# Kernel tuning notes

Hardware: AMD Instinct MI355X
Metric: run time of the kernel (lower is better)

The kernel has to match this reference:

```python
import jax, jax.numpy as jnp
import numpy as np
from jax.scipy.special import xlogy

W_BI = 0.5
W_TRI = 0.5
EPS = 1e-10


def setup_inputs() -> dict:
    key = jax.random.key(0)
    B, L, V = 8, 2048, 512
    logits = jax.random.normal(key, (B, L, V), dtype=jnp.float32)
    return {"logits": logits}


def _safe_normalized_entropy(joint, max_log):
    # 1 - H(joint)/H_max (concentration penalty), fp32-safe
    joint = joint / (joint.sum() + EPS)
    entropy = -xlogy(joint, jnp.clip(joint, EPS, None)).sum()
    return jnp.clip(1.0 - entropy / (max_log + EPS), 0.0, 1.0)


def reference(logits):
    x = jnp.nan_to_num(logits.astype(jnp.float32), nan=0.0, posinf=80.0, neginf=-80.0)
    p = jax.nn.softmax(x, axis=-1)  # (B, L, V)
    B, L, V = p.shape
    max_log_bi = float(np.log(float(V * V)))
    max_log_tri = float(np.log(float(V) ** 3))

    total = jnp.zeros((), dtype=jnp.float32)

    # Bigram joint distribution over (V, V)
    bigram_joint = jnp.einsum('nla,nlb->ab', p[:, :-1, :], p[:, 1:, :])
    total = total + W_BI * _safe_normalized_entropy(bigram_joint, max_log_bi)

    # Trigram: (V,V) bigram part outer-producted with third-position marginal -> (V,V,V)
    bi_part = jnp.einsum('nla,nlb->ab', p[:, :-2, :], p[:, 1:-1, :])
    tri_joint = jnp.einsum('ab,nlc->abc', bi_part, p[:, 2:, :])
    total = total + W_TRI * _safe_normalized_entropy(tri_joint, max_log_tri)

    return jnp.clip(jnp.nan_to_num(total, nan=0.0, posinf=1.0), 0.0, 1.0)
```

## Files before the change

### kernel.cpp

```cpp
#include <hip/hip_runtime.h>
#include <math.h>

#define L_SEQ 2048
#define V 512
#define NROWS 16384
#define LDT 16448
#define NSPLIT 32
#define EPS 1e-10

typedef __bf16 bf16x8 __attribute__((ext_vector_type(8)));
typedef float f32x4 __attribute__((ext_vector_type(4)));

#define PT_OFF  ((size_t)0)
#define GP_OFF  ((size_t)512 * LDT * 2)
#define RB_OFF  (GP_OFF + (size_t)NSPLIT * V * V * 4)
#define M_OFF   (RB_OFF + (size_t)23 * V * 4)
#define PC_OFF  (M_OFF + (size_t)V * 4)

#define GLDS16(g, l) __builtin_amdgcn_global_load_lds( \
    (const __attribute__((address_space(1))) unsigned int*)(g), \
    (__attribute__((address_space(3))) unsigned int*)(l), 16, 0, 0)

__device__ __forceinline__ unsigned short f2bf(float f) {
    unsigned u = __float_as_uint(f);
    unsigned r = (u + 0x7fffu + ((u >> 16) & 1u)) >> 16;
    return (unsigned short)r;
}

__device__ __forceinline__ void softmax_row_bf16(const float* __restrict__ x,
                                                 int lane, unsigned short* out) {
    float4 va = *(const float4*)(x + lane * 4);
    float4 vb = *(const float4*)(x + 256 + lane * 4);
    float v[8] = {va.x, va.y, va.z, va.w, vb.x, vb.y, vb.z, vb.w};
    float e[8];
    float s = 0.0f;
#pragma unroll
    for (int i = 0; i < 8; i++) {
        float xi = fminf(fmaxf(v[i], -80.0f), 80.0f);
        e[i] = __expf(xi);
        s += e[i];
    }
#pragma unroll
    for (int o = 32; o; o >>= 1) s += __shfl_xor(s, o, 64);
    float inv = 1.0f / s;
#pragma unroll
    for (int i = 0; i < 8; i++) out[i] = f2bf(e[i] * inv);
}

__global__ __launch_bounds__(256) void softmaxT_k(const float* __restrict__ in,
                                                  unsigned short* __restrict__ pT,
                                                  float* __restrict__ rb) {
    __shared__ __align__(16) unsigned short sm[32 * 512];
    int t = threadIdx.x;
    int w = t >> 6, lane = t & 63;
    if (blockIdx.x >= 512) {
        int j = blockIdx.x - 512;
        if (w == 0) {
            int r = j < 8 ? j * L_SEQ + L_SEQ - 2
                  : j < 16 ? (j - 8) * L_SEQ + L_SEQ - 1
                  : (j - 15) * L_SEQ;
            unsigned short o[8];
            softmax_row_bf16(in + (size_t)r * V, lane, o);
#pragma unroll
            for (int i = 0; i < 4; i++)
                rb[j * V + lane * 4 + i] = __uint_as_float((unsigned)o[i] << 16);
#pragma unroll
            for (int i = 0; i < 4; i++)
                rb[j * V + 256 + lane * 4 + i] = __uint_as_float((unsigned)o[4 + i] << 16);
        }
        return;
    }
    int k0 = blockIdx.x * 32;
#pragma unroll
    for (int i = 0; i < 8; i++) {
        int rr = w * 8 + i;
        unsigned short o[8];
        softmax_row_bf16(in + (size_t)(k0 + rr) * V, lane, o);
        *(ushort4*)&sm[rr * 512 + lane * 4] = make_ushort4(o[0], o[1], o[2], o[3]);
        *(ushort4*)&sm[rr * 512 + 256 + lane * 4] = make_ushort4(o[4], o[5], o[6], o[7]);
    }
    __syncthreads();
    int cA = 2 * t, cB = cA + 1;
    unsigned u[32];
#pragma unroll
    for (int k = 0; k < 32; k++) u[k] = *(const unsigned*)&sm[k * 512 + cA];
    unsigned oA[16], oB[16];
#pragma unroll
    for (int i = 0; i < 16; i++) {
        unsigned e0 = u[2 * i], e1 = u[2 * i + 1];
        oA[i] = (e0 & 0xffffu) | (e1 << 16);
        oB[i] = (e0 >> 16) | (e1 & 0xffff0000u);
    }
    uint4* dA = (uint4*)(pT + (size_t)cA * LDT + k0);
    uint4* dB = (uint4*)(pT + (size_t)cB * LDT + k0);
#pragma unroll
    for (int i = 0; i < 4; i++) {
        dA[i] = make_uint4(oA[4 * i], oA[4 * i + 1], oA[4 * i + 2], oA[4 * i + 3]);
        dB[i] = make_uint4(oB[4 * i], oB[4 * i + 1], oB[4 * i + 2], oB[4 * i + 3]);
    }
    if (blockIdx.x == 511) {
#pragma unroll
        for (int j = 0; j < 8; j++) {
            *(uint4*)(pT + (size_t)cA * LDT + 16384 + 8 * j) = make_uint4(0, 0, 0, 0);
            *(uint4*)(pT + (size_t)cB * LDT + 16384 + 8 * j) = make_uint4(0, 0, 0, 0);
        }
    }
}

__global__ __launch_bounds__(256) void gemm_k(const unsigned short* __restrict__ pT,
                                              float* __restrict__ gp) {
    __shared__ __align__(16) uint4 ldsA[512];
    __shared__ __align__(16) uint4 ldsB[512];
    int tile = blockIdx.x & 15, split = blockIdx.x >> 4;
    int ta = (tile >> 2) * 128, tb = (tile & 3) * 128;
    int t = threadIdx.x, w = t >> 6, lane = t & 63;
    int l15 = lane & 15, q = lane >> 4;
    int wa = (w & 1) * 64, wb = (w >> 1) * 64;
    int k0base = split * 512;

    f32x4 acc[4][4];
#pragma unroll
    for (int g = 0; g < 4; g++)
#pragma unroll
        for (int h = 0; h < 4; h++) acc[g][h] = (f32x4){0.f, 0.f, 0.f, 0.f};

    int srow = 16 * w + (lane >> 2);
    int qoff = (lane & 3) * 8;
    const size_t rA1 = (size_t)(ta + srow) * LDT;
    const size_t rA2 = (size_t)(ta + 64 + srow) * LDT;
    const size_t rB1 = (size_t)(tb + srow) * LDT;
    const size_t rB2 = (size_t)(tb + 64 + srow) * LDT;

    for (int it = 0; it < 16; it++) {
        int kel = k0base + it * 32 + qoff;
        const unsigned short* gb1 = pT + rB1 + kel;
        const unsigned short* gb2 = pT + rB2 + kel;
        uint4 x1 = *(const uint4*)gb1;
        unsigned y1 = *(const unsigned*)(gb1 + 8);
        uint4 x2 = *(const uint4*)gb2;
        unsigned y2 = *(const unsigned*)(gb2 + 8);
        __syncthreads();
        GLDS16(pT + rA1 + kel, &ldsA[64 * w]);
        GLDS16(pT + rA2 + kel, &ldsA[256 + 64 * w]);
        uint4 s1, s2;
        s1.x = (x1.x >> 16) | (x1.y << 16);
        s1.y = (x1.y >> 16) | (x1.z << 16);
        s1.z = (x1.z >> 16) | (x1.w << 16);
        s1.w = (x1.w >> 16) | (y1 << 16);
        s2.x = (x2.x >> 16) | (x2.y << 16);
        s2.y = (x2.y >> 16) | (x2.z << 16);
        s2.z = (x2.z >> 16) | (x2.w << 16);
        s2.w = (x2.w >> 16) | (y2 << 16);
        ldsB[64 * w + lane] = s1;
        ldsB[256 + 64 * w + lane] = s2;
        __syncthreads();
        bf16x8 af[4], bv[4];
#pragma unroll
        for (int g = 0; g < 4; g++)
            af[g] = __builtin_bit_cast(bf16x8, ldsA[4 * (wa + g * 16 + l15) + q]);
#pragma unroll
        for (int h = 0; h < 4; h++)
            bv[h] = __builtin_bit_cast(bf16x8, ldsB[4 * (wb + h * 16 + l15) + q]);
#pragma unroll
        for (int g = 0; g < 4; g++)
#pragma unroll
            for (int h = 0; h < 4; h++)
                acc[g][h] = __builtin_amdgcn_mfma_f32_16x16x32_bf16(af[g], bv[h], acc[g][h], 0, 0, 0);
    }

    float* og = gp + (size_t)split * V * V;
#pragma unroll
    for (int g = 0; g < 4; g++) {
        int a = ta + wa + g * 16 + q * 4;
#pragma unroll
        for (int h = 0; h < 4; h++) {
            int b = tb + wb + h * 16 + l15;
#pragma unroll
            for (int r = 0; r < 4; r++)
                og[(size_t)(a + r) * V + b] = acc[g][h][r];
        }
    }
}

__global__ __launch_bounds__(256) void reduce_k(const unsigned short* __restrict__ pT,
                                                const float* __restrict__ gp,
                                                const float* __restrict__ rb,
                                                float* __restrict__ m,
                                                double* __restrict__ pc) {
    int bid = blockIdx.x, t = threadIdx.x;
    if (bid < 512) {
        const unsigned short* row = pT + (size_t)bid * LDT;
        float s = 0.0f;
#pragma unroll
        for (int j = 0; j < 8; j++) {
            int g = t + 256 * j;
            uint4 x = *(const uint4*)(row + g * 8);
            float partial = 0.0f;
            unsigned ww[4] = {x.x, x.y, x.z, x.w};
#pragma unroll
            for (int qq = 0; qq < 4; qq++) {
                partial += __uint_as_float(ww[qq] << 16);
                partial += __uint_as_float(ww[qq] & 0xffff0000u);
            }
            if ((g & 255) == 0)
                partial -= __uint_as_float(ww[0] << 16) + __uint_as_float(ww[0] & 0xffff0000u);
            s += partial;
        }
#pragma unroll
        for (int o = 32; o; o >>= 1) s += __shfl_xor(s, o, 64);
        __shared__ float redc[4];
        if ((t & 63) == 0) redc[t >> 6] = s;
        __syncthreads();
        if (t == 0) m[bid] = redc[0] + redc[1] + redc[2] + redc[3];
    } else {
        int idx = (bid - 512) * 256 + t;
        int a = idx >> 9, b = idx & (V - 1);
        double ga = 0, gb2 = 0, gc = 0, gd = 0;
#pragma unroll
        for (int s = 0; s < NSPLIT; s += 4) {
            ga += (double)gp[(size_t)(s + 0) * V * V + idx];
            gb2 += (double)gp[(size_t)(s + 1) * V * V + idx];
            gc += (double)gp[(size_t)(s + 2) * V * V + idx];
            gd += (double)gp[(size_t)(s + 3) * V * V + idx];
        }
        double g = (ga + gb2) + (gc + gd);
        float cross = 0.f, cc = 0.f;
#pragma unroll
        for (int n = 0; n < 7; n++)
            cross = fmaf(rb[(8 + n) * V + a], rb[(16 + n) * V + b], cross);
#pragma unroll
        for (int n = 0; n < 8; n++)
            cc = fmaf(rb[n * V + a], rb[(8 + n) * V + b], cc);
        double g1 = g - (double)cross;
        double g2 = g1 - (double)cc;
        double s1 = g1, t1 = g1 * (double)logf((float)g1);
        double s2 = g2, t2 = g2 * (double)logf((float)g2);
#pragma unroll
        for (int o = 32; o; o >>= 1) {
            s1 += __shfl_xor(s1, o, 64);
            t1 += __shfl_xor(t1, o, 64);
            s2 += __shfl_xor(s2, o, 64);
            t2 += __shfl_xor(t2, o, 64);
        }
        __shared__ double redg[4][4];
        if ((t & 63) == 0) {
            int w = t >> 6;
            redg[w][0] = s1; redg[w][1] = t1; redg[w][2] = s2; redg[w][3] = t2;
        }
        __syncthreads();
        if (t == 0) {
            double* o = pc + (size_t)(bid - 512) * 4;
            o[0] = redg[0][0] + redg[1][0] + redg[2][0] + redg[3][0];
            o[1] = redg[0][1] + redg[1][1] + redg[2][1] + redg[3][1];
            o[2] = redg[0][2] + redg[1][2] + redg[2][2] + redg[3][2];
            o[3] = redg[0][3] + redg[1][3] + redg[2][3] + redg[3][3];
        }
    }
}

__global__ __launch_bounds__(512) void final_k(const float* __restrict__ m,
                                               const double* __restrict__ pc,
                                               float* __restrict__ out) {
    int t = threadIdx.x;
    double s1 = 0, t1 = 0, s2 = 0, t2 = 0;
#pragma unroll
    for (int j = 0; j < 2; j++) {
        const double* q = pc + (size_t)(t + 512 * j) * 4;
        s1 += q[0]; t1 += q[1]; s2 += q[2]; t2 += q[3];
    }
    double mv = (double)m[t];
    double sm = mv;
    double tm = mv * log(mv);
#pragma unroll
    for (int o = 32; o; o >>= 1) {
        sm += __shfl_xor(sm, o, 64);
        tm += __shfl_xor(tm, o, 64);
        s1 += __shfl_xor(s1, o, 64);
        t1 += __shfl_xor(t1, o, 64);
        s2 += __shfl_xor(s2, o, 64);
        t2 += __shfl_xor(t2, o, 64);
    }
    __shared__ double red[6][8];
    if ((t & 63) == 0) {
        int w = t >> 6;
        red[0][w] = sm; red[1][w] = tm;
        red[2][w] = s1; red[3][w] = t1;
        red[4][w] = s2; red[5][w] = t2;
    }
    __syncthreads();
    if (t == 0) {
        double acc[6];
        for (int i = 0; i < 6; i++) {
            acc[i] = 0;
            for (int w = 0; w < 8; w++) acc[i] += red[i][w];
        }
        double Sm = acc[0], Tm = acc[1];
        double S1 = acc[2], T1 = acc[3], S2 = acc[4], T2 = acc[5];
        double D1 = S1 + EPS;
        double Hbi = (log(D1) * S1 - T1) / D1;
        double mlb = log((double)V * (double)V);
        double cbi = 1.0 - Hbi / (mlb + EPS);
        cbi = fmin(fmax(cbi, 0.0), 1.0);
        double S3 = S2 * Sm;
        double D3 = S3 + EPS;
        double Htri = (log(D3) * S3 - (Sm * T2 + S2 * Tm)) / D3;
        double mlt = log((double)V * (double)V * (double)V);
        double ctri = 1.0 - Htri / (mlt + EPS);
        ctri = fmin(fmax(ctri, 0.0), 1.0);
        double tot = 0.5 * cbi + 0.5 * ctri;
        if (!(tot == tot)) tot = 0.0;
        tot = fmin(fmax(tot, 0.0), 1.0);
        out[0] = (float)tot;
    }
}

extern "C" void kernel_launch(void* const* d_in, const int* in_sizes, int n_in,
                              void* d_out, int out_size, void* d_ws, size_t ws_size,
                              hipStream_t stream) {
    (void)in_sizes; (void)n_in; (void)out_size; (void)ws_size;
    const float* logits = (const float*)d_in[0];
    float* out = (float*)d_out;
    char* ws = (char*)d_ws;
    unsigned short* pT = (unsigned short*)(ws + PT_OFF);
    float* gp = (float*)(ws + GP_OFF);
    float* rb = (float*)(ws + RB_OFF);
    float* m = (float*)(ws + M_OFF);
    double* pc = (double*)(ws + PC_OFF);

    softmaxT_k<<<535, 256, 0, stream>>>(logits, pT, rb);
    gemm_k<<<512, 256, 0, stream>>>(pT, gp);
    reduce_k<<<1536, 256, 0, stream>>>(pT, gp, rb, m, pc);
    final_k<<<1, 512, 0, stream>>>(m, pc, out);
}
```

Measured before the change: 114.9 us.

## Fuse column marginal partial sums into softmax and remap GEMM blocks per XCD

The softmax-transpose kernel now also computes per-block partial column sums of the bf16 probabilities, skipping the first two rows of each sequence, and writes them to a new workspace buffer. The reduce kernel combines these 512x512 partials instead of re-reading the whole 16 MB transposed probability matrix, which cuts its marginal-block count from 512 to 16. Separately, the GEMM block-to-(split, tile) mapping is changed so that each XCD handles contiguous K-splits, aiming for better L2 reuse of the A/B panels. The cost is an extra 1 MB write in the softmax kernel and a different floating-point summation order for the marginals.

New measurement: 114.0 us. No clear change (-0.7%).

```diff
diff --git a/kernel.cpp b/kernel.cpp
--- a/kernel.cpp
+++ b/kernel.cpp
@@ -16,6 +16,7 @@
 #define RB_OFF  (GP_OFF + (size_t)NSPLIT * V * V * 4)
 #define M_OFF   (RB_OFF + (size_t)23 * V * 4)
 #define PC_OFF  (M_OFF + (size_t)V * 4)
+#define MP_OFF  (PC_OFF + (size_t)1024 * 4 * 8)
 
 #define GLDS16(g, l) __builtin_amdgcn_global_load_lds( \
     (const __attribute__((address_space(1))) unsigned int*)(g), \
@@ -49,7 +50,8 @@
 
 __global__ __launch_bounds__(256) void softmaxT_k(const float* __restrict__ in,
                                                   unsigned short* __restrict__ pT,
-                                                  float* __restrict__ rb) {
+                                                  float* __restrict__ rb,
+                                                  float* __restrict__ mp) {
     __shared__ __align__(16) unsigned short sm[32 * 512];
     int t = threadIdx.x;
     int w = t >> 6, lane = t & 63;
@@ -84,6 +86,15 @@
     unsigned u[32];
 #pragma unroll
     for (int k = 0; k < 32; k++) u[k] = *(const unsigned*)&sm[k * 512 + cA];
+    bool excl = ((blockIdx.x & 63) == 0);
+    float mA = 0.0f, mB = 0.0f;
+#pragma unroll
+    for (int k = 0; k < 32; k++) {
+        if (excl && k < 2) continue;
+        mA += __uint_as_float(u[k] << 16);
+        mB += __uint_as_float(u[k] & 0xffff0000u);
+    }
+    *(float2*)&mp[(size_t)blockIdx.x * 512 + cA] = make_float2(mA, mB);
     unsigned oA[16], oB[16];
 #pragma unroll
     for (int i = 0; i < 16; i++) {
@@ -111,7 +122,10 @@
                                               float* __restrict__ gp) {
     __shared__ __align__(16) uint4 ldsA[512];
     __shared__ __align__(16) uint4 ldsB[512];
-    int tile = blockIdx.x & 15, split = blockIdx.x >> 4;
+    int b = blockIdx.x;
+    int xcd = b & 7, j = b >> 3;
+    int split = xcd * 4 + (j >> 4);
+    int tile = j & 15;
     int ta = (tile >> 2) * 128, tb = (tile & 3) * 128;
     int t = threadIdx.x, w = t >> 6, lane = t & 63;
     int l15 = lane & 15, q = lane >> 4;
@@ -174,46 +188,38 @@
         int a = ta + wa + g * 16 + q * 4;
 #pragma unroll
         for (int h = 0; h < 4; h++) {
-            int b = tb + wb + h * 16 + l15;
+            int b2 = tb + wb + h * 16 + l15;
 #pragma unroll
             for (int r = 0; r < 4; r++)
-                og[(size_t)(a + r) * V + b] = acc[g][h][r];
-        }
-    }
-}
-
-__global__ __launch_bounds__(256) void reduce_k(const unsigned short* __restrict__ pT,
+                og[(size_t)(a + r) * V + b2] = acc[g][h][r];
+        }
+    }
+}
+
+__global__ __launch_bounds__(256) void reduce_k(const float* __restrict__ mp,
                                                 const float* __restrict__ gp,
                                                 const float* __restrict__ rb,
                                                 float* __restrict__ m,
                                                 double* __restrict__ pc) {
     int bid = blockIdx.x, t = threadIdx.x;
-    if (bid < 512) {
-        const unsigned short* row = pT + (size_t)bid * LDT;
+    if (bid < 16) {
+        int c = bid * 32 + (t & 31);
+        int seg = t >> 5;
         float s = 0.0f;
 #pragma unroll
-        for (int j = 0; j < 8; j++) {
-            int g = t + 256 * j;
-            uint4 x = *(const uint4*)(row + g * 8);
-            float partial = 0.0f;
-            unsigned ww[4] = {x.x, x.y, x.z, x.w};
-#pragma unroll
-            for (int qq = 0; qq < 4; qq++) {
-                partial += __uint_as_float(ww[qq] << 16);
-                partial += __uint_as_float(ww[qq] & 0xffff0000u);
-            }
-            if ((g & 255) == 0)
-                partial -= __uint_as_float(ww[0] << 16) + __uint_as_float(ww[0] & 0xffff0000u);
-            s += partial;
-        }
-#pragma unroll
-        for (int o = 32; o; o >>= 1) s += __shfl_xor(s, o, 64);
-        __shared__ float redc[4];
-        if ((t & 63) == 0) redc[t >> 6] = s;
+        for (int i = 0; i < 64; i++)
+            s += mp[(size_t)(seg * 64 + i) * 512 + c];
+        __shared__ float redm[8][32];
+        redm[seg][t & 31] = s;
         __syncthreads();
-        if (t == 0) m[bid] = redc[0] + redc[1] + redc[2] + redc[3];
+        if (t < 32) {
+            float acc = 0.0f;
+#pragma unroll
+            for (int sgi = 0; sgi < 8; sgi++) acc += redm[sgi][t];
+            m[bid * 32 + t] = acc;
+        }
     } else {
-        int idx = (bid - 512) * 256 + t;
+        int idx = (bid - 16) * 256 + t;
         int a = idx >> 9, b = idx & (V - 1);
         double ga = 0, gb2 = 0, gc = 0, gd = 0;
 #pragma unroll
@@ -249,7 +255,7 @@
         }
         __syncthreads();
         if (t == 0) {
-            double* o = pc + (size_t)(bid - 512) * 4;
+            double* o = pc + (size_t)(bid - 16) * 4;
             o[0] = redg[0][0] + redg[1][0] + redg[2][0] + redg[3][0];
             o[1] = redg[0][1] + redg[1][1] + redg[2][1] + redg[3][1];
             o[2] = redg[0][2] + redg[1][2] + redg[2][2] + redg[3][2];
@@ -326,9 +332,10 @@
     float* rb = (float*)(ws + RB_OFF);
     float* m = (float*)(ws + M_OFF);
     double* pc = (double*)(ws + PC_OFF);
-
-    softmaxT_k<<<535, 256, 0, stream>>>(logits, pT, rb);
+    float* mp = (float*)(ws + MP_OFF);
+
+    softmaxT_k<<<535, 256, 0, stream>>>(logits, pT, rb, mp);
     gemm_k<<<512, 256, 0, stream>>>(pT, gp);
-    reduce_k<<<1536, 256, 0, stream>>>(pT, gp, rb, m, pc);
+    reduce_k<<<1040, 256, 0, stream>>>(mp, gp, rb, m, pc);
     final_k<<<1, 512, 0, stream>>>(m, pc, out);
 }
```
